# Kernel tuning notes

Measured on AMD Instinct MI355X. Metric: run time of the kernel, lower is better.

## Reference

```python
import jax, jax.numpy as jnp
import numpy as np

N_NODES = 200_000
N_EDGES = 6_400_000
N_GRAPHS = 512


def _graph_conv(x, src, dst, W_rel, b_rel, W_root, n_nodes):
    # PyG GraphConv (aggr='add'): lin_rel(sum_{j->i} x_j) + lin_root(x_i)
    agg = jax.ops.segment_sum(x[src], dst, num_segments=n_nodes)  # [N, in]
    return agg @ W_rel.T + b_rel + x @ W_root.T


def setup_inputs() -> dict:
    key = jax.random.key(0)
    ks = jax.random.split(key, 12)
    x = jax.random.normal(ks[0], (N_NODES, 3), dtype=jnp.float32)
    edge_index = jax.random.randint(ks[1], (2, N_EDGES), 0, N_NODES, dtype=jnp.int64)
    batch = jnp.sort(jax.random.randint(ks[2], (N_NODES,), 0, N_GRAPHS, dtype=jnp.int64))

    def xavier(k, shape):
        fan_out, fan_in = shape
        lim = np.sqrt(6.0 / (fan_in + fan_out)).astype(np.float32)
        return jax.random.uniform(k, shape, jnp.float32, -lim, lim)

    return {
        "x": x, "edge_index": edge_index, "batch": batch,
        "W1_rel": xavier(ks[3], (32, 3)),  "b1": jnp.zeros((32,), jnp.float32), "W1_root": xavier(ks[4], (32, 3)),
        "W2_rel": xavier(ks[5], (16, 32)), "b2": jnp.zeros((16,), jnp.float32), "W2_root": xavier(ks[6], (16, 32)),
        "W3_rel": xavier(ks[7], (8, 16)),  "b3": jnp.zeros((8,), jnp.float32),  "W3_root": xavier(ks[8], (8, 16)),
        "W_lin": xavier(ks[9], (1, 8)),    "b_lin": jnp.zeros((1,), jnp.float32),
    }


def reference(x, edge_index, batch,
              W1_rel, b1, W1_root,
              W2_rel, b2, W2_root,
              W3_rel, b3, W3_root,
              W_lin, b_lin):
    src, dst = edge_index[0], edge_index[1]
    h = jax.nn.relu(_graph_conv(x, src, dst, W1_rel, b1, W1_root, N_NODES))
    h = jax.nn.relu(_graph_conv(h, src, dst, W2_rel, b2, W2_root, N_NODES))
    h = jax.nn.relu(_graph_conv(h, src, dst, W3_rel, b3, W3_root, N_NODES))
    pooled = jax.ops.segment_max(h, batch, num_segments=N_GRAPHS)  # [G, 8]
    out = pooled @ W_lin.T + b_lin  # [G, 1]
    return out[:, 0]
```

## Files before the change

### kernel.cpp

```cpp
#include <hip/hip_runtime.h>
#include <hip/hip_fp16.h>

#define N_NODES 200000
#define N_EDGES 6400000
#define N_GRAPHS 512

#define NB1 196
#define CB 1024
#define CHUNK 8192
#define NCH 782
#define NGRP 25
#define CPG 32
#define ST2 512

typedef float vf4 __attribute__((ext_vector_type(4)));
typedef float vf2 __attribute__((ext_vector_type(2)));
typedef unsigned vu2 __attribute__((ext_vector_type(2)));

__device__ __forceinline__ unsigned ntload_u(const unsigned* p) {
  return __builtin_nontemporal_load(p);
}
__device__ __forceinline__ int ntload_i(const int* p) { return __builtin_nontemporal_load(p); }
__device__ __forceinline__ float ntload_f(const float* p) {
  return __builtin_nontemporal_load(p);
}
__device__ __forceinline__ float2 ntload_f2(const float* p) {
  vf2 v = __builtin_nontemporal_load((const vf2*)p);
  return make_float2(v.x, v.y);
}
__device__ __forceinline__ void ntstore_u2(unsigned* p, uint2 v) {
  vu2 t = {v.x, v.y};
  __builtin_nontemporal_store(t, (vu2*)p);
}
__device__ __forceinline__ void ntstore_f2(float* p, float2 v) {
  vf2 t = {v.x, v.y};
  __builtin_nontemporal_store(t, (vf2*)p);
}
__device__ __forceinline__ void ntstore_f4(float* p, float4 v) {
  vf4 t = {v.x, v.y, v.z, v.w};
  __builtin_nontemporal_store(t, (vf4*)p);
}
__device__ __forceinline__ void ntstore_u(unsigned* p, unsigned v) {
  __builtin_nontemporal_store(v, p);
}


__global__ __launch_bounds__(256) void count_kernel(const int* __restrict__ dst,
                                                    unsigned short* __restrict__ H) {
  __shared__ unsigned hist[4][NB1];
  int t = threadIdx.x, w = t >> 6;
  for (int i = t; i < 4 * NB1; i += 256) ((unsigned*)hist)[i] = 0;
  __syncthreads();
  int c = blockIdx.x;
  long e0 = (long)c * CHUNK;
  long rem = (long)N_EDGES - e0;
  int n = rem > CHUNK ? CHUNK : (int)rem;
  for (int i = t; i < n; i += 256) atomicAdd(&hist[w][dst[e0 + i] >> 10], 1u);
  __syncthreads();
  for (int b = t; b < NB1; b += 256)
    H[(size_t)c * NB1 + b] =
        (unsigned short)(hist[0][b] + hist[1][b] + hist[2][b] + hist[3][b]);
}

__global__ __launch_bounds__(256) void scan_bins1_kernel(unsigned short* __restrict__ H,
                                                         unsigned* __restrict__ P) {
  int b = blockIdx.x * 256 + threadIdx.x;
  int g = blockIdx.y;
  if (b >= NB1) return;
  int c0 = g * CPG, c1 = min(NCH, (g + 1) * CPG);
  unsigned run = 0;
  for (int c = c0; c < c1; c++) {
    unsigned t = H[(size_t)c * NB1 + b];
    H[(size_t)c * NB1 + b] = (unsigned short)run;
    run += t;
  }
  P[(size_t)g * NB1 + b] = run;
}

__global__ __launch_bounds__(256) void scan_bins2_kernel(unsigned* __restrict__ P,
                                                         unsigned* __restrict__ bucketTotal) {
  int b = blockIdx.x * 256 + threadIdx.x;
  if (b >= NB1) return;
  unsigned run = 0;
  for (int g = 0; g < NGRP; g++) {
    unsigned t = P[(size_t)g * NB1 + b];
    P[(size_t)g * NB1 + b] = run;
    run += t;
  }
  bucketTotal[b] = run;
}

__global__ __launch_bounds__(256) void scan_total_kernel(const unsigned* __restrict__ bucketTotal,
                                                         unsigned* __restrict__ bucketStart) {
  __shared__ unsigned partial[256];
  int t = threadIdx.x;
  unsigned v = (t < NB1) ? bucketTotal[t] : 0u;
  partial[t] = v;
  __syncthreads();
  for (int off = 1; off < 256; off <<= 1) {
    unsigned add = (t >= off) ? partial[t - off] : 0u;
    __syncthreads();
    partial[t] += add;
    __syncthreads();
  }
  if (t < NB1) bucketStart[t] = partial[t] - v;
  if (t == 0) bucketStart[NB1] = N_EDGES;
}

__global__ __launch_bounds__(256) void scatter_sorted_kernel(
    const int* __restrict__ src, const int* __restrict__ dst,
    const unsigned short* __restrict__ H, const unsigned* __restrict__ P,
    const unsigned* __restrict__ bucketStart, unsigned* __restrict__ packed) {
  __shared__ unsigned ssort[CHUNK];
  __shared__ unsigned char sbort[CHUNK];
  __shared__ unsigned histw[4][NB1];
  __shared__ unsigned curw[4][NB1];
  __shared__ unsigned gbase[NB1];
  __shared__ unsigned partial[256];
  int t = threadIdx.x, w = t >> 6;
  int c = blockIdx.x;
  int g = c / CPG;
  long e0 = (long)c * CHUNK;
  long rem = (long)N_EDGES - e0;
  int n = rem > CHUNK ? CHUNK : (int)rem;
  for (int i = t; i < 4 * NB1; i += 256) ((unsigned*)histw)[i] = 0;
  __syncthreads();
  for (int i = t; i < n; i += 256) atomicAdd(&histw[w][dst[e0 + i] >> 10], 1u);
  __syncthreads();
  unsigned tot = 0, h0 = 0, h1 = 0, h2 = 0, h3 = 0;
  if (t < NB1) {
    h0 = histw[0][t]; h1 = histw[1][t]; h2 = histw[2][t]; h3 = histw[3][t];
    tot = h0 + h1 + h2 + h3;
  }
  partial[t] = tot;
  __syncthreads();
  for (int off = 1; off < 256; off <<= 1) {
    unsigned add = (t >= off) ? partial[t - off] : 0u;
    __syncthreads();
    partial[t] += add;
    __syncthreads();
  }
  if (t < NB1) {
    unsigned ex = partial[t] - tot;
    unsigned r = ex;
    curw[0][t] = r; r += h0;
    curw[1][t] = r; r += h1;
    curw[2][t] = r; r += h2;
    curw[3][t] = r;
    gbase[t] = bucketStart[t] + P[(size_t)g * NB1 + t] + (unsigned)H[(size_t)c * NB1 + t] - ex;
  }
  __syncthreads();
  for (int i = t; i < n; i += 256) {
    int d = dst[e0 + i], s = src[e0 + i];
    int b = d >> 10;
    unsigned r = atomicAdd(&curw[w][b], 1u);
    ssort[r] = ((unsigned)s << 10) | (unsigned)(d & 1023);
    sbort[r] = (unsigned char)b;
  }
  __syncthreads();
  for (int j = t; j < n; j += 256) packed[gbase[sbort[j]] + j] = ssort[j];
}

__global__ __launch_bounds__(ST2) void sort2_kernel(const unsigned* __restrict__ packedA,
                                                    const unsigned* __restrict__ bucketStart,
                                                    unsigned* __restrict__ packedB,
                                                    unsigned* __restrict__ nodeStart) {
  __shared__ unsigned hist[CB];
  __shared__ unsigned cur[CB];
  __shared__ unsigned partial[ST2];
  int t = threadIdx.x, b = blockIdx.x;
  unsigned s0 = bucketStart[b], s1 = bucketStart[b + 1];
  int n = (int)(s1 - s0);
  for (int i = t; i < CB; i += ST2) hist[i] = 0;
  __syncthreads();
  for (int i = t; i < n; i += ST2) atomicAdd(&hist[packedA[s0 + i] & 1023u], 1u);
  __syncthreads();
  unsigned a0 = hist[2 * t], a1 = hist[2 * t + 1];
  unsigned sum = a0 + a1;
  partial[t] = sum;
  __syncthreads();
  for (int off = 1; off < ST2; off <<= 1) {
    unsigned add = (t >= off) ? partial[t - off] : 0u;
    __syncthreads();
    partial[t] += add;
    __syncthreads();
  }
  unsigned run = partial[t] - sum;
  __syncthreads();
  hist[2 * t] = run;
  cur[2 * t] = run;
  hist[2 * t + 1] = run + a0;
  cur[2 * t + 1] = run + a0;
  __syncthreads();
  int gnode = b * CB;
  for (int k = t; k < CB; k += ST2) {
    int gn = gnode + k;
    if (gn <= N_NODES) nodeStart[gn] = s0 + hist[k];
  }
  for (int i = t; i < n; i += ST2) {
    unsigned v = packedA[s0 + i];
    unsigned pos = atomicAdd(&cur[v & 1023u], 1u);
    packedB[s0 + pos] = v >> 10;
  }
}

__global__ __launch_bounds__(256) void xpad_kernel(const float* __restrict__ x,
                                                   float4* __restrict__ xp) {
  int n = blockIdx.x * 256 + threadIdx.x;
  if (n >= N_NODES) return;
  xp[n] = make_float4(x[3 * n], x[3 * n + 1], x[3 * n + 2], 0.f);
}

__device__ __forceinline__ void half8_unpack(uint4 g, float* f) {
  const __half2* h2 = reinterpret_cast<const __half2*>(&g);
#pragma unroll
  for (int j = 0; j < 4; j++) {
    float2 fj = __half22float2(h2[j]);
    f[2 * j] = fj.x;
    f[2 * j + 1] = fj.y;
  }
}

__global__ __launch_bounds__(256) void layer1_kernel(
    const unsigned* __restrict__ packed, const unsigned* __restrict__ nodeStart,
    const float4* __restrict__ xp,
    const float* __restrict__ W1_rel, const float* __restrict__ b1,
    const float* __restrict__ W1_root,
    const float* __restrict__ W2_rel, const float* __restrict__ W2_root,
    unsigned* __restrict__ t2h, float* __restrict__ r2) {
  __shared__ float sW1rel[96], sW1root[96], sb1[32], sW2rel[512], sW2root[512];
  __shared__ float plds[256 * 4];
  for (int i = threadIdx.x; i < 96; i += 256) { sW1rel[i] = W1_rel[i]; sW1root[i] = W1_root[i]; }
  for (int i = threadIdx.x; i < 32; i += 256) sb1[i] = b1[i];
  for (int i = threadIdx.x; i < 512; i += 256) { sW2rel[i] = W2_rel[i]; sW2root[i] = W2_root[i]; }
  __syncthreads();
  int t = threadIdx.x, ln = t >> 2, part = t & 3;
  int node = blockIdx.x * 64 + ln;
  unsigned s1v = ntload_u(&nodeStart[node + 1]);
  float a0 = 0.f, a1 = 0.f, a2 = 0.f;
  for (unsigned base = ntload_u(&nodeStart[node]) + part; base < s1v; base += 16) {
    unsigned i1 = base + 4, i2 = base + 8, i3 = base + 12;
    unsigned e0 = ntload_u(&packed[base]);
    unsigned e1 = ntload_u(&packed[i1]);
    unsigned e2 = ntload_u(&packed[i2]);
    unsigned e3 = ntload_u(&packed[i3]);
    float4 g0 = xp[e0], g1 = xp[e1], g2 = xp[e2], g3 = xp[e3];
    float m1 = (i1 < s1v) ? 1.f : 0.f;
    float m2 = (i2 < s1v) ? 1.f : 0.f;
    float m3 = (i3 < s1v) ? 1.f : 0.f;
    a0 += g0.x + m1 * g1.x + m2 * g2.x + m3 * g3.x;
    a1 += g0.y + m1 * g1.y + m2 * g2.y + m3 * g3.y;
    a2 += g0.z + m1 * g1.z + m2 * g2.z + m3 * g3.z;
  }
  plds[t * 4] = a0; plds[t * 4 + 1] = a1; plds[t * 4 + 2] = a2;
  __syncthreads();
  int pb = ln * 16;
  float A0 = plds[pb] + plds[pb + 4] + plds[pb + 8] + plds[pb + 12];
  float A1 = plds[pb + 1] + plds[pb + 5] + plds[pb + 9] + plds[pb + 13];
  float A2 = plds[pb + 2] + plds[pb + 6] + plds[pb + 10] + plds[pb + 14];
  float4 xv = xp[node];
  float h[32];
#pragma unroll
  for (int k = 0; k < 32; k++) {
    float v = sW1rel[3 * k] * A0 + sW1rel[3 * k + 1] * A1 + sW1rel[3 * k + 2] * A2 +
              sW1root[3 * k] * xv.x + sW1root[3 * k + 1] * xv.y + sW1root[3 * k + 2] * xv.z +
              sb1[k];
    h[k] = fmaxf(v, 0.f);
  }
  int jb = part * 4;
  float tv[4], rv[4];
#pragma unroll
  for (int j = 0; j < 4; j++) {
    float acc = 0.f, accr = 0.f;
#pragma unroll
    for (int k = 0; k < 32; k++) {
      acc += sW2rel[32 * (jb + j) + k] * h[k];
      accr += sW2root[32 * (jb + j) + k] * h[k];
    }
    tv[j] = acc;
    rv[j] = accr;
  }
  __half2 p0 = __halves2half2(__float2half_rn(tv[0]), __float2half_rn(tv[1]));
  __half2 p1 = __halves2half2(__float2half_rn(tv[2]), __float2half_rn(tv[3]));
  ntstore_u2(&t2h[(size_t)node * 8 + part * 2], make_uint2(*(unsigned*)&p0, *(unsigned*)&p1));
  ntstore_f4(&r2[(size_t)node * 16 + jb], make_float4(rv[0], rv[1], rv[2], rv[3]));
}

__global__ __launch_bounds__(256) void layer2_kernel(
    const unsigned* __restrict__ packed, const unsigned* __restrict__ nodeStart,
    const uint4* __restrict__ t2h4, const float* __restrict__ r2,
    const float* __restrict__ b2,
    const float* __restrict__ W3_rel, const float* __restrict__ W3_root,
    unsigned* __restrict__ t3h, float* __restrict__ r3) {
  __shared__ float sW3rel[128], sW3root[128], sb2[16];
  __shared__ float plds[256 * 9];
  __shared__ float hlds[32 * 16];
  for (int i = threadIdx.x; i < 128; i += 256) { sW3rel[i] = W3_rel[i]; sW3root[i] = W3_root[i]; }
  if (threadIdx.x < 16) sb2[threadIdx.x] = b2[threadIdx.x];
  __syncthreads();
  int t = threadIdx.x, ln = t >> 3, p = t & 7;
  int node = blockIdx.x * 32 + ln;
  int half = p & 1;
  unsigned s1v = ntload_u(&nodeStart[node + 1]);
  float acc[8];
#pragma unroll
  for (int j = 0; j < 8; j++) acc[j] = 0.f;
  for (unsigned base = ntload_u(&nodeStart[node]) + (p >> 1); base < s1v; base += 16) {
    unsigned i1 = base + 4, i2 = base + 8, i3 = base + 12;
    unsigned e0 = ntload_u(&packed[base]);
    unsigned e1 = ntload_u(&packed[i1]);
    unsigned e2 = ntload_u(&packed[i2]);
    unsigned e3 = ntload_u(&packed[i3]);
    uint4 g0 = t2h4[(size_t)e0 * 2 + half];
    uint4 g1 = t2h4[(size_t)e1 * 2 + half];
    uint4 g2 = t2h4[(size_t)e2 * 2 + half];
    uint4 g3 = t2h4[(size_t)e3 * 2 + half];
    float m1 = (i1 < s1v) ? 1.f : 0.f;
    float m2 = (i2 < s1v) ? 1.f : 0.f;
    float m3 = (i3 < s1v) ? 1.f : 0.f;
    float f0[8], f1[8], f2[8], f3[8];
    half8_unpack(g0, f0);
    half8_unpack(g1, f1);
    half8_unpack(g2, f2);
    half8_unpack(g3, f3);
#pragma unroll
    for (int j = 0; j < 8; j++)
      acc[j] += f0[j] + m1 * f1[j] + m2 * f2[j] + m3 * f3[j];
  }
#pragma unroll
  for (int j = 0; j < 8; j++) plds[t * 9 + j] = acc[j];
  __syncthreads();
  {
    float2 rv = ntload_f2(&r2[(size_t)node * 16 + 2 * p]);
    float hv[2];
#pragma unroll
    for (int k2 = 0; k2 < 2; k2++) {
      int f = 2 * p + k2;
      int fh = f >> 3, fi = f & 7;
      int q0 = (ln * 8 + fh) * 9 + fi;
      float s = plds[q0] + plds[q0 + 18] + plds[q0 + 36] + plds[q0 + 54];
      hv[k2] = s + sb2[f] + (k2 == 0 ? rv.x : rv.y);
    }
    hlds[ln * 16 + 2 * p] = fmaxf(hv[0], 0.f);
    hlds[ln * 16 + 2 * p + 1] = fmaxf(hv[1], 0.f);
  }
  __syncthreads();
  const float* W = (p < 4) ? sW3rel : sW3root;
  int rbase = (p < 4) ? 2 * p : 2 * (p - 4);
  float o0 = 0.f, o1 = 0.f;
#pragma unroll
  for (int k = 0; k < 16; k++) {
    float hv = hlds[ln * 16 + k];
    o0 += W[16 * rbase + k] * hv;
    o1 += W[16 * (rbase + 1) + k] * hv;
  }
  if (p < 4) {
    __half2 pk = __halves2half2(__float2half_rn(o0), __float2half_rn(o1));
    ntstore_u(&t3h[(size_t)node * 4 + p], *(unsigned*)&pk);
  } else {
    ntstore_f2(&r3[(size_t)node * 8 + rbase], make_float2(o0, o1));
  }
}

__global__ __launch_bounds__(256) void layer3_kernel(
    const unsigned* __restrict__ packed, const unsigned* __restrict__ nodeStart,
    const uint4* __restrict__ t3h4, const float* __restrict__ r3,
    const float* __restrict__ b3,
    const int* __restrict__ batch, unsigned* __restrict__ pooled) {
  __shared__ float plds[256 * 9];
  __shared__ float sb3[8];
  __shared__ int sgid[32];
  if (threadIdx.x < 8) sb3[threadIdx.x] = b3[threadIdx.x];
  __syncthreads();
  int t = threadIdx.x, ln = t >> 3, p = t & 7;
  int node = blockIdx.x * 32 + ln;
  unsigned s1v = ntload_u(&nodeStart[node + 1]);
  float acc[8];
#pragma unroll
  for (int j = 0; j < 8; j++) acc[j] = 0.f;
  for (unsigned base = ntload_u(&nodeStart[node]) + p; base < s1v; base += 32) {
    unsigned i1 = base + 8, i2 = base + 16, i3 = base + 24;
    unsigned e0 = ntload_u(&packed[base]);
    unsigned e1 = ntload_u(&packed[i1]);
    unsigned e2 = ntload_u(&packed[i2]);
    unsigned e3 = ntload_u(&packed[i3]);
    uint4 g0 = t3h4[e0];
    uint4 g1 = t3h4[e1];
    uint4 g2 = t3h4[e2];
    uint4 g3 = t3h4[e3];
    float m1 = (i1 < s1v) ? 1.f : 0.f;
    float m2 = (i2 < s1v) ? 1.f : 0.f;
    float m3 = (i3 < s1v) ? 1.f : 0.f;
    float f0[8], f1[8], f2[8], f3[8];
    half8_unpack(g0, f0);
    half8_unpack(g1, f1);
    half8_unpack(g2, f2);
    half8_unpack(g3, f3);
#pragma unroll
    for (int j = 0; j < 8; j++)
      acc[j] += f0[j] + m1 * f1[j] + m2 * f2[j] + m3 * f3[j];
  }
#pragma unroll
  for (int j = 0; j < 8; j++) plds[t * 9 + j] = acc[j];
  __syncthreads();
  int gg = ntload_i(&batch[node]);
  int q0 = ln * 72 + p;
  float v = plds[q0] + plds[q0 + 9] + plds[q0 + 18] + plds[q0 + 27] +
            plds[q0 + 36] + plds[q0 + 45] + plds[q0 + 54] + plds[q0 + 63];
  float h = fmaxf(v + sb3[p] + ntload_f(&r3[(size_t)node * 8 + p]), 0.f);
  __syncthreads();
  plds[ln * 9 + p] = h;
  if (p == 0) sgid[ln] = gg;
  __syncthreads();
  if (t < 8) {
    int gcur = sgid[0];
    float m = plds[t];
    for (int l = 1; l < 32; l++) {
      int g2 = sgid[l];
      float hv = plds[l * 9 + t];
      if (g2 != gcur) {
        atomicMax(&pooled[8 * gcur + t], __float_as_uint(m));
        gcur = g2;
        m = hv;
      } else {
        m = fmaxf(m, hv);
      }
    }
    atomicMax(&pooled[8 * gcur + t], __float_as_uint(m));
  }
}

__global__ __launch_bounds__(256) void final_kernel(
    const unsigned* __restrict__ pooled, const float* __restrict__ W_lin,
    const float* __restrict__ b_lin, float* __restrict__ out) {
  int g = blockIdx.x * blockDim.x + threadIdx.x;
  if (g >= N_GRAPHS) return;
  float acc = b_lin[0];
#pragma unroll
  for (int f = 0; f < 8; f++) acc += __uint_as_float(pooled[8 * g + f]) * W_lin[f];
  out[g] = acc;
}

extern "C" void kernel_launch(void* const* d_in, const int* in_sizes, int n_in,
                              void* d_out, int out_size, void* d_ws, size_t ws_size,
                              hipStream_t stream) {
  const float* x = (const float*)d_in[0];
  const int* ei = (const int*)d_in[1];
  const int* src = ei;
  const int* dst = ei + N_EDGES;
  const int* batch = (const int*)d_in[2];
  const float* W1_rel = (const float*)d_in[3];
  const float* b1 = (const float*)d_in[4];
  const float* W1_root = (const float*)d_in[5];
  const float* W2_rel = (const float*)d_in[6];
  const float* b2 = (const float*)d_in[7];
  const float* W2_root = (const float*)d_in[8];
  const float* W3_rel = (const float*)d_in[9];
  const float* b3 = (const float*)d_in[10];
  const float* W3_root = (const float*)d_in[11];
  const float* W_lin = (const float*)d_in[12];
  const float* b_lin = (const float*)d_in[13];
  float* out = (float*)d_out;

  char* ws = (char*)d_ws;
  unsigned* packedA = (unsigned*)(ws + 0);
  float* r2 = (float*)(ws + 0);
  float* r3 = (float*)(ws + 12800000);
  unsigned* t3h = (unsigned*)(ws + 19200000);
  float4* xpad = (float4*)(ws + 22400000);
  unsigned short* H = (unsigned short*)(ws + 25600000);
  unsigned* packedB = (unsigned*)(ws + 25600000);
  unsigned* t2h = (unsigned*)(ws + 51200128);
  unsigned* pooled = (unsigned*)(ws + 57600128);
  unsigned* bucketStart = (unsigned*)(ws + 57616512);
  unsigned* bucketTotal = (unsigned*)(ws + 57629016);
  unsigned* P = (unsigned*)(ws + 57641516);
  unsigned* nodeStart = (unsigned*)(ws + 57954016);

  hipMemsetAsync(pooled, 0, N_GRAPHS * 8 * sizeof(unsigned), stream);
  hipMemsetAsync(packedB + N_EDGES, 0, 128, stream);

  count_kernel<<<NCH, 256, 0, stream>>>(dst, H);
  scan_bins1_kernel<<<dim3((NB1 + 255) / 256, NGRP), 256, 0, stream>>>(H, P);
  scan_bins2_kernel<<<(NB1 + 255) / 256, 256, 0, stream>>>(P, bucketTotal);
  scan_total_kernel<<<1, 256, 0, stream>>>(bucketTotal, bucketStart);
  scatter_sorted_kernel<<<NCH, 256, 0, stream>>>(src, dst, H, P, bucketStart, packedA);
  sort2_kernel<<<NB1, ST2, 0, stream>>>(packedA, bucketStart, packedB, nodeStart);
  xpad_kernel<<<(N_NODES + 255) / 256, 256, 0, stream>>>(x, xpad);

  layer1_kernel<<<N_NODES / 64, 256, 0, stream>>>(packedB, nodeStart, xpad,
                                                  W1_rel, b1, W1_root, W2_rel, W2_root, t2h, r2);
  layer2_kernel<<<N_NODES / 32, 256, 0, stream>>>(packedB, nodeStart, (const uint4*)t2h, r2, b2,
                                                  W3_rel, W3_root, t3h, r3);
  layer3_kernel<<<N_NODES / 32, 256, 0, stream>>>(packedB, nodeStart, (const uint4*)t3h, r3, b3,
                                                  batch, pooled);
  final_kernel<<<(N_GRAPHS + 255) / 256, 256, 0, stream>>>(pooled, W_lin, b_lin, out);
}
```

Before: 442.7 us.

## Split second sort pass into coarse sub-bucket scatter plus LDS-local fine sort

The single 196-block second-level counting sort over 1024-node buckets is replaced by two passes. First, a 1024-thread kernel scatters each bucket into 16 sub-buckets of 64 nodes. Then 3136 blocks each sort their sub-bucket entirely in shared memory and write it out coalesced. This is meant to fix the poor occupancy and scattered global writes of the old per-bucket sort. It costs an extra read/write pass over the edge array. It also relies on a fixed LDS capacity (3072) per 64-node sub-bucket, which holds only for roughly uniform edge degrees.

```diff
diff --git a/kernel.cpp b/kernel.cpp
--- a/kernel.cpp
+++ b/kernel.cpp
@@ -7,11 +7,13 @@
 
 #define NB1 196
 #define CB 1024
+#define NSB 16
+#define NFB (NB1 * NSB)
 #define CHUNK 8192
 #define NCH 782
 #define NGRP 25
 #define CPG 32
-#define ST2 512
+#define SCAP 3072
 
 typedef float vf4 __attribute__((ext_vector_type(4)));
 typedef float vf2 __attribute__((ext_vector_type(2)));
@@ -107,10 +109,10 @@
   if (t == 0) bucketStart[NB1] = N_EDGES;
 }
 
-__global__ __launch_bounds__(256) void scatter_sorted_kernel(
+__global__ __launch_bounds__(256) void scatterA_kernel(
     const int* __restrict__ src, const int* __restrict__ dst,
     const unsigned short* __restrict__ H, const unsigned* __restrict__ P,
-    const unsigned* __restrict__ bucketStart, unsigned* __restrict__ packed) {
+    const unsigned* __restrict__ bucketStart, unsigned* __restrict__ X1) {
   __shared__ unsigned ssort[CHUNK];
   __shared__ unsigned char sbort[CHUNK];
   __shared__ unsigned histw[4][NB1];
@@ -158,50 +160,83 @@
     sbort[r] = (unsigned char)b;
   }
   __syncthreads();
-  for (int j = t; j < n; j += 256) packed[gbase[sbort[j]] + j] = ssort[j];
-}
-
-__global__ __launch_bounds__(ST2) void sort2_kernel(const unsigned* __restrict__ packedA,
-                                                    const unsigned* __restrict__ bucketStart,
+  for (int j = t; j < n; j += 256) X1[gbase[sbort[j]] + j] = ssort[j];
+}
+
+__global__ __launch_bounds__(1024) void scatterB_kernel(
+    const unsigned* __restrict__ X1, const unsigned* __restrict__ bucketStart,
+    unsigned* __restrict__ X2, unsigned* __restrict__ fineStart) {
+  __shared__ unsigned histw[16][NSB];
+  __shared__ unsigned binstart[NSB + 1];
+  __shared__ unsigned cur[NSB];
+  int t = threadIdx.x, w = t >> 6, b = blockIdx.x;
+  unsigned cs0 = bucketStart[b], cs1 = bucketStart[b + 1];
+  int n = (int)(cs1 - cs0);
+  if (t < 16 * NSB) ((unsigned*)histw)[t] = 0;
+  __syncthreads();
+  for (int i = t; i < n; i += 1024)
+    atomicAdd(&histw[w][(X1[cs0 + i] >> 6) & 15u], 1u);
+  __syncthreads();
+  if (t == 0) {
+    unsigned run = 0;
+    for (int k = 0; k < NSB; k++) {
+      binstart[k] = run;
+      unsigned tot = 0;
+      for (int ww = 0; ww < 16; ww++) tot += histw[ww][k];
+      run += tot;
+    }
+    binstart[NSB] = run;
+  }
+  __syncthreads();
+  if (t < NSB) {
+    fineStart[b * NSB + t] = cs0 + binstart[t];
+    cur[t] = binstart[t];
+  }
+  if (b == NB1 - 1 && t == 0) fineStart[NFB] = cs1;
+  __syncthreads();
+  for (int i = t; i < n; i += 1024) {
+    unsigned v = X1[cs0 + i];
+    unsigned pos = atomicAdd(&cur[(v >> 6) & 15u], 1u);
+    X2[cs0 + pos] = v;
+  }
+}
+
+__global__ __launch_bounds__(256) void sort2_kernel(const unsigned* __restrict__ X2,
+                                                    const unsigned* __restrict__ fineStart,
                                                     unsigned* __restrict__ packedB,
                                                     unsigned* __restrict__ nodeStart) {
-  __shared__ unsigned hist[CB];
-  __shared__ unsigned cur[CB];
-  __shared__ unsigned partial[ST2];
+  __shared__ unsigned buf[SCAP];
+  __shared__ unsigned buf2[SCAP];
+  __shared__ unsigned hist[64], base[64], cur[64];
   int t = threadIdx.x, b = blockIdx.x;
-  unsigned s0 = bucketStart[b], s1 = bucketStart[b + 1];
+  unsigned s0 = fineStart[b], s1 = fineStart[b + 1];
   int n = (int)(s1 - s0);
-  for (int i = t; i < CB; i += ST2) hist[i] = 0;
-  __syncthreads();
-  for (int i = t; i < n; i += ST2) atomicAdd(&hist[packedA[s0 + i] & 1023u], 1u);
-  __syncthreads();
-  unsigned a0 = hist[2 * t], a1 = hist[2 * t + 1];
-  unsigned sum = a0 + a1;
-  partial[t] = sum;
-  __syncthreads();
-  for (int off = 1; off < ST2; off <<= 1) {
-    unsigned add = (t >= off) ? partial[t - off] : 0u;
-    __syncthreads();
-    partial[t] += add;
-    __syncthreads();
-  }
-  unsigned run = partial[t] - sum;
-  __syncthreads();
-  hist[2 * t] = run;
-  cur[2 * t] = run;
-  hist[2 * t + 1] = run + a0;
-  cur[2 * t + 1] = run + a0;
-  __syncthreads();
-  int gnode = b * CB;
-  for (int k = t; k < CB; k += ST2) {
-    int gn = gnode + k;
-    if (gn <= N_NODES) nodeStart[gn] = s0 + hist[k];
-  }
-  for (int i = t; i < n; i += ST2) {
-    unsigned v = packedA[s0 + i];
-    unsigned pos = atomicAdd(&cur[v & 1023u], 1u);
-    packedB[s0 + pos] = v >> 10;
-  }
+  if (t < 64) hist[t] = 0;
+  for (int i = t; i < n; i += 256) buf[i] = ntload_u(&X2[s0 + i]);
+  __syncthreads();
+  for (int i = t; i < n; i += 256) atomicAdd(&hist[buf[i] & 63u], 1u);
+  __syncthreads();
+  if (t == 0) {
+    unsigned run = 0;
+    for (int k = 0; k < 64; k++) {
+      unsigned v = hist[k];
+      base[k] = run;
+      cur[k] = run;
+      run += v;
+    }
+  }
+  __syncthreads();
+  if (t < 64) {
+    int gn = b * 64 + t;
+    if (gn <= N_NODES) nodeStart[gn] = s0 + base[t];
+  }
+  for (int i = t; i < n; i += 256) {
+    unsigned p = buf[i];
+    unsigned pos = atomicAdd(&cur[p & 63u], 1u);
+    buf2[pos] = p >> 10;
+  }
+  __syncthreads();
+  for (int i = t; i < n; i += 256) ntstore_u(&packedB[s0 + i], buf2[i]);
 }
 
 __global__ __launch_bounds__(256) void xpad_kernel(const float* __restrict__ x,
@@ -463,18 +498,20 @@
   float* out = (float*)d_out;
 
   char* ws = (char*)d_ws;
-  unsigned* packedA = (unsigned*)(ws + 0);
+  unsigned* X2 = (unsigned*)(ws + 0);
   float* r2 = (float*)(ws + 0);
   float* r3 = (float*)(ws + 12800000);
   unsigned* t3h = (unsigned*)(ws + 19200000);
   float4* xpad = (float4*)(ws + 22400000);
-  unsigned short* H = (unsigned short*)(ws + 25600000);
+  unsigned* X1 = (unsigned*)(ws + 25600000);
   unsigned* packedB = (unsigned*)(ws + 25600000);
   unsigned* t2h = (unsigned*)(ws + 51200128);
+  unsigned short* H = (unsigned short*)(ws + 51200128);
+  unsigned* P = (unsigned*)(ws + 51506672);
+  unsigned* bucketTotal = (unsigned*)(ws + 51526272);
+  unsigned* bucketStart = (unsigned*)(ws + 51527056);
+  unsigned* fineStart = (unsigned*)(ws + 51527844);
   unsigned* pooled = (unsigned*)(ws + 57600128);
-  unsigned* bucketStart = (unsigned*)(ws + 57616512);
-  unsigned* bucketTotal = (unsigned*)(ws + 57629016);
-  unsigned* P = (unsigned*)(ws + 57641516);
   unsigned* nodeStart = (unsigned*)(ws + 57954016);
 
   hipMemsetAsync(pooled, 0, N_GRAPHS * 8 * sizeof(unsigned), stream);
@@ -484,8 +521,9 @@
   scan_bins1_kernel<<<dim3((NB1 + 255) / 256, NGRP), 256, 0, stream>>>(H, P);
   scan_bins2_kernel<<<(NB1 + 255) / 256, 256, 0, stream>>>(P, bucketTotal);
   scan_total_kernel<<<1, 256, 0, stream>>>(bucketTotal, bucketStart);
-  scatter_sorted_kernel<<<NCH, 256, 0, stream>>>(src, dst, H, P, bucketStart, packedA);
-  sort2_kernel<<<NB1, ST2, 0, stream>>>(packedA, bucketStart, packedB, nodeStart);
+  scatterA_kernel<<<NCH, 256, 0, stream>>>(src, dst, H, P, bucketStart, X1);
+  scatterB_kernel<<<NB1, 1024, 0, stream>>>(X1, bucketStart, X2, fineStart);
+  sort2_kernel<<<NFB, 256, 0, stream>>>(X2, fineStart, packedB, nodeStart);
   xpad_kernel<<<(N_NODES + 255) / 256, 256, 0, stream>>>(x, xpad);
 
   layer1_kernel<<<N_NODES / 64, 256, 0, stream>>>(packedB, nodeStart, xpad,
```

After: 422.8 us. -4.5%, faster.
